# Performance work log

Measured on AMD Instinct MI355X. Metric: run time of the kernel, lower is better.

Reference implementation:

```python
import jax, jax.numpy as jnp
import numpy as np

B, T, E, D, H = 4, 2048, 512, 768, 12
DH = D // H  # 64
S = T + E


def _heads(x, W, b):
    # x: [B, L, D] -> [B, H, L, DH]
    y = x @ W.T + b
    return y.reshape(y.shape[0], y.shape[1], H, DH).transpose(0, 2, 1, 3)


def setup_inputs() -> dict:
    key = jax.random.key(0)
    ks = jax.random.split(key, 16)
    p = lambda k, shape: (jax.random.normal(k, shape, dtype=jnp.float32) * 0.02)
    inp = {
        'token_hidden_states': jax.random.normal(ks[0], (B, T, D), dtype=jnp.float32),
        'entity_hidden_states': jax.random.normal(ks[1], (B, E, D), dtype=jnp.float32),
        'attention_mask': jnp.zeros((B, 1, 1, S), dtype=jnp.float32),
        'query_pos': jax.random.normal(ks[2], (B, E, D), dtype=jnp.float32),
        'Wq': p(ks[3], (D, D)), 'bq': jnp.zeros((D,), jnp.float32),
        'Wk': p(ks[4], (D, D)), 'bk': jnp.zeros((D,), jnp.float32),
        'Wv': p(ks[5], (D, D)), 'bv': jnp.zeros((D,), jnp.float32),
        'Weq': p(ks[6], (D, D)), 'beq': jnp.zeros((D,), jnp.float32),
        'Wek': p(ks[7], (D, D)), 'bek': jnp.zeros((D,), jnp.float32),
        'Wev': p(ks[8], (D, D)), 'bev': jnp.zeros((D,), jnp.float32),
    }
    return inp


def reference(token_hidden_states, entity_hidden_states, attention_mask, query_pos,
              Wq, bq, Wk, bk, Wv, bv, Weq, beq, Wek, bek, Wev, bev):
    pae = (entity_hidden_states + query_pos) * 0.5  # pos-aware entity states
    # Projections into heads: [B, H, L, DH]
    q_w = _heads(token_hidden_states, Wq, bq)
    q_e = _heads(pae, Weq, beq)
    k_w = _heads(token_hidden_states, Wk, bk)
    k_e = _heads(pae, Wek, bek)
    v_w = _heads(token_hidden_states, Wv, bv)
    v_e = _heads(entity_hidden_states, Wev, bev)
    # Concatenating Q and K along the sequence axis reproduces exactly the
    # four-block (w2w, w2e, e2w, e2e) score matrix of the original module.
    q = jnp.concatenate([q_w, q_e], axis=2)  # [B, H, S, DH]
    k = jnp.concatenate([k_w, k_e], axis=2)
    v = jnp.concatenate([v_w, v_e], axis=2)
    scores = jnp.einsum('bhqd,bhkd->bhqk', q, k) / jnp.sqrt(jnp.float32(DH))
    scores = scores + attention_mask  # additive mask, broadcast over heads/queries
    probs = jax.nn.softmax(scores, axis=-1)  # dropout prob = 0 (eval)
    ctx = jnp.einsum('bhqk,bhkd->bhqd', probs, v)  # [B, H, S, DH]
    ctx = ctx.transpose(0, 2, 1, 3).reshape(B, S, D)
    return ctx[:, :T, :], ctx[:, T:, :]
```

## Files before the change

### kernel.cpp

```cpp
#include <hip/hip_runtime.h>
#include <stdint.h>

constexpr int Bn = 4, Tn = 2048, En = 512, Dn = 768, Hn = 12, DHn = 64, Sn = 2560;

typedef __bf16 bf16x8 __attribute__((ext_vector_type(8)));
typedef float f32x4 __attribute__((ext_vector_type(4)));

#define MFMA16x16x32 __builtin_amdgcn_mfma_f32_16x16x32_bf16

#define GLOAD_LDS16(g, l)                                                        \
  __builtin_amdgcn_global_load_lds((const __attribute__((address_space(1))) uint32_t*)(g), \
                                   (__attribute__((address_space(3))) uint32_t*)(l), 16, 0, 0)

#define QSCALE 0.1803368843f
#define LOG2E  1.4426950409f

__device__ __forceinline__ unsigned short f2bf(float f) {
  union { float f; uint32_t u; } c;
  c.f = f;
  return (unsigned short)((c.u + 0x7fffu + ((c.u >> 16) & 1u)) >> 16);
}

__global__ __launch_bounds__(256) void prep_all(
    const float* __restrict__ tok, const float* __restrict__ ent,
    const float* __restrict__ qp, const float* __restrict__ mask,
    const float* __restrict__ w0, const float* __restrict__ w1, const float* __restrict__ w2,
    const float* __restrict__ w3, const float* __restrict__ w4, const float* __restrict__ w5,
    unsigned short* __restrict__ Xw, unsigned short* __restrict__ Xq,
    unsigned short* __restrict__ Xe, unsigned short* __restrict__ Wc,
    float* __restrict__ maskS)
{
  const int TOK4 = Bn * Tn * Dn / 4;
  const int ENT4 = Bn * En * Dn / 4;
  const int W4 = Dn * Dn / 4;
  int i = blockIdx.x * 256 + threadIdx.x;
  if (i < TOK4) {
    float4 v = ((const float4*)tok)[i];
    ushort4 o = { f2bf(v.x), f2bf(v.y), f2bf(v.z), f2bf(v.w) };
    ((ushort4*)Xw)[i] = o;
    return;
  }
  i -= TOK4;
  if (i < ENT4) {
    float4 e = ((const float4*)ent)[i];
    float4 q = ((const float4*)qp)[i];
    ushort4 p = { f2bf((e.x + q.x) * 0.5f), f2bf((e.y + q.y) * 0.5f),
                  f2bf((e.z + q.z) * 0.5f), f2bf((e.w + q.w) * 0.5f) };
    ushort4 x = { f2bf(e.x), f2bf(e.y), f2bf(e.z), f2bf(e.w) };
    ((ushort4*)Xq)[i] = p;
    ((ushort4*)Xe)[i] = x;
    return;
  }
  i -= ENT4;
  if (i < 6 * W4) {
    int wi = i / W4, off = i - wi * W4;
    const float* src = (wi == 0) ? w0 : (wi == 1) ? w1 : (wi == 2) ? w2
                     : (wi == 3) ? w3 : (wi == 4) ? w4 : w5;
    float4 v = ((const float4*)src)[off];
    ushort4 o = { f2bf(v.x), f2bf(v.y), f2bf(v.z), f2bf(v.w) };
    ((ushort4*)Wc)[i] = o;
    return;
  }
  i -= 6 * W4;
  {
    float4 v = ((const float4*)mask)[i];
    float4 o = { v.x * LOG2E, v.y * LOG2E, v.z * LOG2E, v.w * LOG2E };
    ((float4*)maskS)[i] = o;
  }
}

__global__ __launch_bounds__(256, 2) void proj_gemm(
    const unsigned short* __restrict__ Xw_, const unsigned short* __restrict__ Xq_,
    const unsigned short* __restrict__ Xe_, const unsigned short* __restrict__ Wc,
    const float* __restrict__ b0, const float* __restrict__ b1, const float* __restrict__ b2,
    const float* __restrict__ b3, const float* __restrict__ b4, const float* __restrict__ b5,
    unsigned short* __restrict__ Qb, unsigned short* __restrict__ Kb, unsigned short* __restrict__ Vtb)
{
  const int z = blockIdx.z;
  const bool tokseg = (blockIdx.x < 64);
  const int m0 = tokseg ? blockIdx.x * 128 : (blockIdx.x - 64) * 128;
  const int widx = tokseg ? z : z + 3;
  const unsigned short* X = tokseg ? Xw_ : ((z == 2) ? Xe_ : Xq_);
  const unsigned short* W = Wc + (size_t)widx * Dn * Dn;
  const float* bias = (widx == 0) ? b0 : (widx == 1) ? b1 : (widx == 2) ? b2
                    : (widx == 3) ? b3 : (widx == 4) ? b4 : b5;
  const bool swap = (z != 2);
  const float oscale = (z == 0) ? QSCALE : 1.0f;
  const int batch = tokseg ? (m0 >> 11) : (m0 >> 9);
  const int sbase = tokseg ? (m0 & 2047) : (Tn + (m0 & 511));

  const int t = threadIdx.x;
  const int lane = t & 63, wave = t >> 6;
  const int l15 = lane & 15, g = lane >> 4;
  const int n0 = blockIdx.y * 128;

  __shared__ __align__(16) unsigned short ldsX[2][4096];
  __shared__ __align__(16) unsigned short ldsW[2][4096];

  f32x4 acc[4][4];
#pragma unroll
  for (int a = 0; a < 4; ++a)
#pragma unroll
    for (int b = 0; b < 4; ++b) acc[a][b] = (f32x4){0.f, 0.f, 0.f, 0.f};

  auto stage = [&](int buf, int k0) {
#pragma unroll
    for (int i = 0; i < 2; ++i) {
      int idx0 = i * 256 + wave * 64;
      int r = (idx0 + lane) >> 2;
      int ko = k0 + ((lane & 3) << 3);
      GLOAD_LDS16(X + (size_t)(m0 + r) * Dn + ko, &ldsX[buf][idx0 * 8]);
      GLOAD_LDS16(W + (size_t)(n0 + r) * Dn + ko, &ldsW[buf][idx0 * 8]);
    }
  };

  stage(0, 0);
  __syncthreads();

  const int aw = wave >> 1, bw = wave & 1;

  for (int ks = 0; ks < 24; ++ks) {
    int cur = ks & 1;
    if (ks < 23) stage(cur ^ 1, (ks + 1) * 32);
    const unsigned short* tX = ldsX[cur];
    const unsigned short* tW = ldsW[cur];
    const unsigned short* tA = swap ? tW : tX;
    const unsigned short* tB = swap ? tX : tW;
    bf16x8 af[4], bfr[4];
#pragma unroll
    for (int f = 0; f < 4; ++f) {
      int r = aw * 64 + f * 16 + l15;
      af[f] = *(const bf16x8*)(tA + r * 32 + (g << 3));
    }
#pragma unroll
    for (int f = 0; f < 4; ++f) {
      int r = bw * 64 + f * 16 + l15;
      bfr[f] = *(const bf16x8*)(tB + r * 32 + (g << 3));
    }
    __builtin_amdgcn_s_setprio(1);
#pragma unroll
    for (int mf = 0; mf < 4; ++mf)
#pragma unroll
      for (int nf = 0; nf < 4; ++nf)
        acc[mf][nf] = MFMA16x16x32(af[mf], bfr[nf], acc[mf][nf], 0, 0, 0);
    __builtin_amdgcn_s_setprio(0);
    __syncthreads();
  }

  if (swap) {
    unsigned short* outb = (z == 0) ? Qb : Kb;
#pragma unroll
    for (int mf = 0; mf < 4; ++mf) {
      int n = n0 + aw * 64 + mf * 16 + 4 * g;
      float4 b4 = *(const float4*)(bias + n);
      int h = n >> 6, dh0 = n & 63;
#pragma unroll
      for (int nf = 0; nf < 4; ++nf) {
        int s = sbase + bw * 64 + nf * 16 + l15;
        f32x4 a = acc[mf][nf];
        ushort4 o = { f2bf((a[0] + b4.x) * oscale), f2bf((a[1] + b4.y) * oscale),
                      f2bf((a[2] + b4.z) * oscale), f2bf((a[3] + b4.w) * oscale) };
        *(ushort4*)(outb + (((size_t)batch * Hn + h) * Sn + s) * DHn + dh0) = o;
      }
    }
  } else {
#pragma unroll
    for (int nf = 0; nf < 4; ++nf) {
      int n = n0 + bw * 64 + nf * 16 + l15;
      float bv = bias[n];
      int h = n >> 6, dh = n & 63;
      size_t vtrow = ((size_t)batch * Hn + h) * DHn + dh;
#pragma unroll
      for (int mf = 0; mf < 4; ++mf) {
        int s = sbase + aw * 64 + mf * 16 + 4 * g;
        f32x4 a = acc[mf][nf];
        ushort4 o = { f2bf(a[0] + bv), f2bf(a[1] + bv), f2bf(a[2] + bv), f2bf(a[3] + bv) };
        *(ushort4*)(Vtb + vtrow * Sn + s) = o;
      }
    }
  }
}

template<int NSPLIT>
__global__ __launch_bounds__(256, 4) void attn_kernel(
    const unsigned short* __restrict__ Qb, const unsigned short* __restrict__ Kb,
    const unsigned short* __restrict__ Vtb, const float* __restrict__ maskS,
    float* __restrict__ out, float* __restrict__ ctxP, float* __restrict__ Lbuf)
{
  const int t = threadIdx.x, lane = t & 63, wave = t >> 6;
  const int l15 = lane & 15, g = lane >> 4;

  const int nx = 20 * NSPLIT;
  const int bid = blockIdx.y * nx + blockIdx.x;
  const int perx = (48 * nx) >> 3;
  const int swz = (bid & 7) * perx + (bid >> 3);
  const int bx = swz % nx, by = swz / nx;
  const int bb = by / Hn, h = by % Hn;
  const int qt = (NSPLIT == 2) ? (bx >> 1) : bx;
  const int half = (NSPLIT == 2) ? (bx & 1) : 0;
  const int qw = qt * 128 + wave * 32;
  const int kvbase = half * (Sn / NSPLIT);
  const int nchunk = Sn / 64 / NSPLIT;

  __shared__ __align__(16) unsigned short Klds[2][4096];
  __shared__ __align__(16) unsigned short Vlds[2][4096];

  const size_t headQ = ((size_t)bb * Hn + h) * Sn * DHn;
  const size_t headV = ((size_t)bb * Hn + h) * DHn * Sn;

  auto stage = [&](int buf, int c) {
    const int kv0 = kvbase + c * 64;
#pragma unroll
    for (int i = 0; i < 2; ++i) {
      int idx0 = i * 256 + wave * 64;
      int r = (idx0 + lane) >> 3;
      int ssl = ((lane & 7) ^ (r & 7)) << 3;
      GLOAD_LDS16(Kb + headQ + (size_t)(kv0 + r) * DHn + ssl, &Klds[buf][idx0 * 8]);
      GLOAD_LDS16(Vtb + headV + (size_t)r * Sn + kv0 + ssl, &Vlds[buf][idx0 * 8]);
    }
  };

  bf16x8 qf[2][2];
#pragma unroll
  for (int i = 0; i < 2; ++i)
#pragma unroll
    for (int kq = 0; kq < 2; ++kq)
      qf[i][kq] = *(const bf16x8*)(Qb + headQ + (size_t)(qw + i * 16 + l15) * DHn + kq * 32 + g * 8);

  const int l7 = l15 & 7;
  int koff[2], voff[2][2];
#pragma unroll
  for (int kq = 0; kq < 2; ++kq)
    koff[kq] = l15 * 128 + (((kq * 4 + g) ^ l7) << 4);
#pragma unroll
  for (int ksv = 0; ksv < 2; ++ksv)
#pragma unroll
    for (int hf = 0; hf < 2; ++hf)
      voff[ksv][hf] = l15 * 128 + (((4 * ksv + 2 * hf + (g >> 1)) ^ l7) << 4) + (g & 1) * 8;

  bf16x8 ones;
#pragma unroll
  for (int j = 0; j < 8; ++j) ones[j] = (l15 == 0) ? (__bf16)1.0f : (__bf16)0.0f;

  f32x4 ctx[2][4];
  f32x4 ctxl[2];
#pragma unroll
  for (int i = 0; i < 2; ++i) {
#pragma unroll
    for (int d = 0; d < 4; ++d) ctx[i][d] = (f32x4){0.f, 0.f, 0.f, 0.f};
    ctxl[i] = (f32x4){0.f, 0.f, 0.f, 0.f};
  }

  const char* KBp = (const char*)Klds;
  const char* VBp = (const char*)Vlds;
  const float* maskB = maskS + (size_t)bb * Sn;

  auto compute = [&](const int buf, const int c) {
    const int kv0 = kvbase + c * 64;
    const char* KB = KBp + buf * 8192;
    const char* VB = VBp + buf * 8192;

    f32x4 mvv[4];
#pragma unroll
    for (int kvf = 0; kvf < 4; ++kvf) {
      float4 mv = *(const float4*)(maskB + kv0 + kvf * 16 + g * 4);
      mvv[kvf] = (f32x4){mv.x, mv.y, mv.z, mv.w};
    }

    f32x4 sacc[2][4];
#pragma unroll
    for (int kvf = 0; kvf < 4; ++kvf) {
      bf16x8 kf0 = *(const bf16x8*)(KB + kvf * 2048 + koff[0]);
      bf16x8 kf1 = *(const bf16x8*)(KB + kvf * 2048 + koff[1]);
      __builtin_amdgcn_s_setprio(1);
      f32x4 s0 = MFMA16x16x32(kf0, qf[0][0], mvv[kvf], 0, 0, 0);
      sacc[0][kvf] = MFMA16x16x32(kf1, qf[0][1], s0, 0, 0, 0);
      f32x4 s1 = MFMA16x16x32(kf0, qf[1][0], mvv[kvf], 0, 0, 0);
      sacc[1][kvf] = MFMA16x16x32(kf1, qf[1][1], s1, 0, 0, 0);
      __builtin_amdgcn_s_setprio(0);
    }

    bf16x8 pb[2][2];
#pragma unroll
    for (int i = 0; i < 2; ++i)
#pragma unroll
      for (int ksv = 0; ksv < 2; ++ksv)
#pragma unroll
        for (int r = 0; r < 4; ++r) {
          pb[i][ksv][r]     = (__bf16)__builtin_amdgcn_exp2f(sacc[i][2 * ksv][r]);
          pb[i][ksv][4 + r] = (__bf16)__builtin_amdgcn_exp2f(sacc[i][2 * ksv + 1][r]);
        }

#pragma unroll
    for (int ksv = 0; ksv < 2; ++ksv) {
#pragma unroll
      for (int df = 0; df < 4; ++df) {
        union { uint64_t u[2]; bf16x8 v; } vv;
        vv.u[0] = *(const uint64_t*)(VB + df * 2048 + voff[ksv][0]);
        vv.u[1] = *(const uint64_t*)(VB + df * 2048 + voff[ksv][1]);
        __builtin_amdgcn_s_setprio(1);
        ctx[0][df] = MFMA16x16x32(vv.v, pb[0][ksv], ctx[0][df], 0, 0, 0);
        ctx[1][df] = MFMA16x16x32(vv.v, pb[1][ksv], ctx[1][df], 0, 0, 0);
        __builtin_amdgcn_s_setprio(0);
      }
      ctxl[0] = MFMA16x16x32(ones, pb[0][ksv], ctxl[0], 0, 0, 0);
      ctxl[1] = MFMA16x16x32(ones, pb[1][ksv], ctxl[1], 0, 0, 0);
    }
  };

  stage(0, 0);

  for (int c = 0; c < nchunk; c += 2) {
    __syncthreads();
    stage(1, c + 1);
    compute(0, c);
    __syncthreads();
    if (c + 2 < nchunk) stage(0, c + 2);
    compute(1, c + 1);
  }

#pragma unroll
  for (int i = 0; i < 2; ++i) {
    float lsum = __shfl(ctxl[i][0], l15);
    int q = qw + i * 16 + l15;
    size_t rowoff;
    if (q < Tn) rowoff = ((size_t)bb * Tn + q) * Dn;
    else        rowoff = (size_t)Bn * Tn * Dn + ((size_t)bb * En + (q - Tn)) * Dn;
    if (NSPLIT == 1) {
      float inv = 1.0f / lsum;
#pragma unroll
      for (int df = 0; df < 4; ++df) {
        int d = h * DHn + df * 16 + 4 * g;
        float4 o = { ctx[i][df][0] * inv, ctx[i][df][1] * inv, ctx[i][df][2] * inv, ctx[i][df][3] * inv };
        *(float4*)(out + rowoff + d) = o;
      }
    } else {
      if (g == 0)
        Lbuf[(size_t)half * (Bn * Hn * Sn) + ((size_t)bb * Hn + h) * Sn + q] = lsum;
      float* obase = half ? ctxP : out;
#pragma unroll
      for (int df = 0; df < 4; ++df) {
        int d = h * DHn + df * 16 + 4 * g;
        float4 o = { ctx[i][df][0], ctx[i][df][1], ctx[i][df][2], ctx[i][df][3] };
        *(float4*)(obase + rowoff + d) = o;
      }
    }
  }
}

__global__ __launch_bounds__(256) void combine_kernel(
    float* __restrict__ out, const float* __restrict__ ctxP, const float* __restrict__ Lbuf)
{
  const int N4 = Bn * Sn * Dn / 4;
  const int BTD4 = Bn * Tn * Dn / 4;
  const int L1off = Bn * Hn * Sn;
  for (int idx = blockIdx.x * 256 + threadIdx.x; idx < N4; idx += gridDim.x * 256) {
    int r = idx / 192;
    int d4 = idx - r * 192;
    int hh = d4 >> 4;
    int b, q;
    if (idx < BTD4) { b = r >> 11; q = r & 2047; }
    else { int r2 = r - Bn * Tn; b = r2 >> 9; q = Tn + (r2 & 511); }
    int li = (b * Hn + hh) * Sn + q;
    float inv = 1.0f / (Lbuf[li] + Lbuf[L1off + li]);
    float4 o = ((const float4*)out)[idx];
    float4 p = ((const float4*)ctxP)[idx];
    float4 res = { (o.x + p.x) * inv, (o.y + p.y) * inv,
                   (o.z + p.z) * inv, (o.w + p.w) * inv };
    ((float4*)out)[idx] = res;
  }
}

extern "C" void kernel_launch(void* const* d_in, const int* in_sizes, int n_in,
                              void* d_out, int out_size, void* d_ws, size_t ws_size,
                              hipStream_t stream) {
  (void)in_sizes; (void)n_in; (void)out_size;
  const float* tok  = (const float*)d_in[0];
  const float* ent  = (const float*)d_in[1];
  const float* mask = (const float*)d_in[2];
  const float* qpos = (const float*)d_in[3];
  const float* Wq = (const float*)d_in[4];  const float* bq = (const float*)d_in[5];
  const float* Wk = (const float*)d_in[6];  const float* bk = (const float*)d_in[7];
  const float* Wv = (const float*)d_in[8];  const float* bv = (const float*)d_in[9];
  const float* Weq = (const float*)d_in[10]; const float* beq = (const float*)d_in[11];
  const float* Wek = (const float*)d_in[12]; const float* bek = (const float*)d_in[13];
  const float* Wev = (const float*)d_in[14]; const float* bev = (const float*)d_in[15];
  float* out = (float*)d_out;

  unsigned short* ws = (unsigned short*)d_ws;
  const size_t headN = (size_t)Bn * Hn * Sn * DHn;
  unsigned short* Qb  = ws;
  unsigned short* Kb  = Qb + headN;
  unsigned short* Vtb = Kb + headN;
  unsigned short* Xw  = Vtb + headN;
  unsigned short* Xq  = Xw + (size_t)Bn * Tn * Dn;
  unsigned short* Xe  = Xq + (size_t)Bn * En * Dn;
  unsigned short* Wc  = Xe + (size_t)Bn * En * Dn;

  const size_t ctxPoff  = (size_t)3 * headN * 2;
  const size_t ctxPsz   = (size_t)Bn * Hn * Sn * DHn * 4;
  const size_t lbufoff  = ctxPoff + ctxPsz;
  const size_t lbufsz   = (size_t)2 * Bn * Hn * Sn * 4;
  const size_t masksoff = lbufoff + lbufsz;
  const size_t NEED_SPLIT = masksoff + (size_t)Bn * Sn * 4;
  const bool split = (ws_size >= NEED_SPLIT);

  float* ctxP = (float*)((char*)d_ws + ctxPoff);
  float* Lbuf = (float*)((char*)d_ws + lbufoff);
  float* maskS = split ? (float*)((char*)d_ws + masksoff)
                       : (float*)(Wc + 6 * (size_t)Dn * Dn);

  const int TOK4 = Bn * Tn * Dn / 4;
  const int ENT4 = Bn * En * Dn / 4;
  const int W4 = Dn * Dn / 4;
  const int MSK4 = Bn * Sn / 4;
  const int total4 = TOK4 + ENT4 + 6 * W4 + MSK4;
  prep_all<<<dim3((total4 + 255) / 256), 256, 0, stream>>>(
      tok, ent, qpos, mask, Wq, Wk, Wv, Weq, Wek, Wev, Xw, Xq, Xe, Wc, maskS);

  proj_gemm<<<dim3(80, Dn / 128, 3), 256, 0, stream>>>(
      Xw, Xq, Xe, Wc, bq, bk, bv, beq, bek, bev, Qb, Kb, Vtb);

  if (split) {
    attn_kernel<2><<<dim3(40, Bn * Hn), 256, 0, stream>>>(Qb, Kb, Vtb, maskS, out, ctxP, Lbuf);
    combine_kernel<<<dim3(2048), 256, 0, stream>>>(out, ctxP, Lbuf);
  } else {
    attn_kernel<1><<<dim3(20, Bn * Hn), 256, 0, stream>>>(Qb, Kb, Vtb, maskS, out, ctxP, Lbuf);
  }
}
```

Measured before the change: 179.6 us.

## Load V directly from global into registers and sum softmax denominators in VALU

V tiles are no longer staged through LDS. Each lane now reads its V fragments straight from global memory into registers at the start of each chunk, which halves LDS usage and the async copies per stage. The row-sum of the exponentials is now built with scalar adds plus two cross-lane shuffles instead of extra MFMAs against a ones vector. Occupancy hint drops from 4 to 3 blocks per CU to leave room for the extra registers. The trade-off is more global-memory latency exposed per chunk, and possibly uncoalesced 8-byte V loads, in exchange for less LDS traffic and fewer MFMAs.

```diff
diff --git a/kernel.cpp b/kernel.cpp
--- a/kernel.cpp
+++ b/kernel.cpp
@@ -182,7 +182,7 @@
 }
 
 template<int NSPLIT>
-__global__ __launch_bounds__(256, 4) void attn_kernel(
+__global__ __launch_bounds__(256, 3) void attn_kernel(
     const unsigned short* __restrict__ Qb, const unsigned short* __restrict__ Kb,
     const unsigned short* __restrict__ Vtb, const float* __restrict__ maskS,
     float* __restrict__ out, float* __restrict__ ctxP, float* __restrict__ Lbuf)
@@ -190,7 +190,8 @@
   const int t = threadIdx.x, lane = t & 63, wave = t >> 6;
   const int l15 = lane & 15, g = lane >> 4;
 
-  const int nx = 20 * NSPLIT;
+  const int QT = Sn / 128;
+  const int nx = QT * NSPLIT;
   const int bid = blockIdx.y * nx + blockIdx.x;
   const int perx = (48 * nx) >> 3;
   const int swz = (bid & 7) * perx + (bid >> 3);
@@ -203,7 +204,6 @@
   const int nchunk = Sn / 64 / NSPLIT;
 
   __shared__ __align__(16) unsigned short Klds[2][4096];
-  __shared__ __align__(16) unsigned short Vlds[2][4096];
 
   const size_t headQ = ((size_t)bb * Hn + h) * Sn * DHn;
   const size_t headV = ((size_t)bb * Hn + h) * DHn * Sn;
@@ -216,7 +216,6 @@
       int r = (idx0 + lane) >> 3;
       int ssl = ((lane & 7) ^ (r & 7)) << 3;
       GLOAD_LDS16(Kb + headQ + (size_t)(kv0 + r) * DHn + ssl, &Klds[buf][idx0 * 8]);
-      GLOAD_LDS16(Vtb + headV + (size_t)r * Sn + kv0 + ssl, &Vlds[buf][idx0 * 8]);
     }
   };
 
@@ -228,83 +227,83 @@
       qf[i][kq] = *(const bf16x8*)(Qb + headQ + (size_t)(qw + i * 16 + l15) * DHn + kq * 32 + g * 8);
 
   const int l7 = l15 & 7;
-  int koff[2], voff[2][2];
+  int koff[2];
 #pragma unroll
   for (int kq = 0; kq < 2; ++kq)
     koff[kq] = l15 * 128 + (((kq * 4 + g) ^ l7) << 4);
-#pragma unroll
-  for (int ksv = 0; ksv < 2; ++ksv)
-#pragma unroll
-    for (int hf = 0; hf < 2; ++hf)
-      voff[ksv][hf] = l15 * 128 + (((4 * ksv + 2 * hf + (g >> 1)) ^ l7) << 4) + (g & 1) * 8;
-
-  bf16x8 ones;
-#pragma unroll
-  for (int j = 0; j < 8; ++j) ones[j] = (l15 == 0) ? (__bf16)1.0f : (__bf16)0.0f;
+
+  const unsigned short* vbase = Vtb + headV + (size_t)l15 * Sn + 4 * g;
 
   f32x4 ctx[2][4];
-  f32x4 ctxl[2];
+  float lacc[2];
 #pragma unroll
   for (int i = 0; i < 2; ++i) {
 #pragma unroll
     for (int d = 0; d < 4; ++d) ctx[i][d] = (f32x4){0.f, 0.f, 0.f, 0.f};
-    ctxl[i] = (f32x4){0.f, 0.f, 0.f, 0.f};
+    lacc[i] = 0.f;
   }
 
   const char* KBp = (const char*)Klds;
-  const char* VBp = (const char*)Vlds;
   const float* maskB = maskS + (size_t)bb * Sn;
 
   auto compute = [&](const int buf, const int c) {
     const int kv0 = kvbase + c * 64;
     const char* KB = KBp + buf * 8192;
-    const char* VB = VBp + buf * 8192;
-
-    f32x4 mvv[4];
+
+    uint64_t vld[2][4][2];
+#pragma unroll
+    for (int ksv = 0; ksv < 2; ++ksv)
+#pragma unroll
+      for (int df = 0; df < 4; ++df) {
+        const unsigned short* p = vbase + (size_t)(df * 16) * Sn + kv0 + ksv * 32;
+        vld[ksv][df][0] = *(const uint64_t*)p;
+        vld[ksv][df][1] = *(const uint64_t*)(p + 16);
+      }
+
+    f32x4 sacc[2][4];
 #pragma unroll
     for (int kvf = 0; kvf < 4; ++kvf) {
       float4 mv = *(const float4*)(maskB + kv0 + kvf * 16 + g * 4);
-      mvv[kvf] = (f32x4){mv.x, mv.y, mv.z, mv.w};
-    }
-
-    f32x4 sacc[2][4];
-#pragma unroll
-    for (int kvf = 0; kvf < 4; ++kvf) {
+      f32x4 mvv = (f32x4){mv.x, mv.y, mv.z, mv.w};
       bf16x8 kf0 = *(const bf16x8*)(KB + kvf * 2048 + koff[0]);
       bf16x8 kf1 = *(const bf16x8*)(KB + kvf * 2048 + koff[1]);
       __builtin_amdgcn_s_setprio(1);
-      f32x4 s0 = MFMA16x16x32(kf0, qf[0][0], mvv[kvf], 0, 0, 0);
+      f32x4 s0 = MFMA16x16x32(kf0, qf[0][0], mvv, 0, 0, 0);
       sacc[0][kvf] = MFMA16x16x32(kf1, qf[0][1], s0, 0, 0, 0);
-      f32x4 s1 = MFMA16x16x32(kf0, qf[1][0], mvv[kvf], 0, 0, 0);
+      f32x4 s1 = MFMA16x16x32(kf0, qf[1][0], mvv, 0, 0, 0);
       sacc[1][kvf] = MFMA16x16x32(kf1, qf[1][1], s1, 0, 0, 0);
       __builtin_amdgcn_s_setprio(0);
     }
 
     bf16x8 pb[2][2];
 #pragma unroll
-    for (int i = 0; i < 2; ++i)
+    for (int i = 0; i < 2; ++i) {
+      float ls = 0.f;
 #pragma unroll
       for (int ksv = 0; ksv < 2; ++ksv)
 #pragma unroll
         for (int r = 0; r < 4; ++r) {
-          pb[i][ksv][r]     = (__bf16)__builtin_amdgcn_exp2f(sacc[i][2 * ksv][r]);
-          pb[i][ksv][4 + r] = (__bf16)__builtin_amdgcn_exp2f(sacc[i][2 * ksv + 1][r]);
+          float e0 = __builtin_amdgcn_exp2f(sacc[i][2 * ksv][r]);
+          float e1 = __builtin_amdgcn_exp2f(sacc[i][2 * ksv + 1][r]);
+          pb[i][ksv][r]     = (__bf16)e0;
+          pb[i][ksv][4 + r] = (__bf16)e1;
+          ls += e0 + e1;
         }
+      lacc[i] += ls;
+    }
 
 #pragma unroll
     for (int ksv = 0; ksv < 2; ++ksv) {
 #pragma unroll
       for (int df = 0; df < 4; ++df) {
         union { uint64_t u[2]; bf16x8 v; } vv;
-        vv.u[0] = *(const uint64_t*)(VB + df * 2048 + voff[ksv][0]);
-        vv.u[1] = *(const uint64_t*)(VB + df * 2048 + voff[ksv][1]);
+        vv.u[0] = vld[ksv][df][0];
+        vv.u[1] = vld[ksv][df][1];
         __builtin_amdgcn_s_setprio(1);
         ctx[0][df] = MFMA16x16x32(vv.v, pb[0][ksv], ctx[0][df], 0, 0, 0);
         ctx[1][df] = MFMA16x16x32(vv.v, pb[1][ksv], ctx[1][df], 0, 0, 0);
         __builtin_amdgcn_s_setprio(0);
       }
-      ctxl[0] = MFMA16x16x32(ones, pb[0][ksv], ctxl[0], 0, 0, 0);
-      ctxl[1] = MFMA16x16x32(ones, pb[1][ksv], ctxl[1], 0, 0, 0);
     }
   };
 
@@ -321,7 +320,9 @@
 
 #pragma unroll
   for (int i = 0; i < 2; ++i) {
-    float lsum = __shfl(ctxl[i][0], l15);
+    float lsum = lacc[i];
+    lsum += __shfl_xor(lsum, 16);
+    lsum += __shfl_xor(lsum, 32);
     int q = qw + i * 16 + l15;
     size_t rowoff;
     if (q < Tn) rowoff = ((size_t)bb * Tn + q) * Dn;
```

After: 432.1 us. 141% more time.
